# Kernel tuning notes

Hardware: AMD Instinct MI355X
Metric: run time of the kernel (lower is better)

The kernel has to match this reference:

```python
import jax, jax.numpy as jnp
import numpy as np

B, N_GENES, N_SETS, G = 256, 10000, 1000, 128   # batch, input_dim, output_dim, geneset_size
H1, H2 = 64, 32                                  # hidden_dims
EPS = 1e-5                                       # BatchNorm1d eps


def _batchnorm(h, gamma, beta):
    # BatchNorm1d in training mode: biased batch stats over the batch axis
    mean = jnp.mean(h, axis=0, keepdims=True)
    var = jnp.mean(jnp.square(h - mean), axis=0, keepdims=True)
    return (h - mean) * jax.lax.rsqrt(var + EPS) * gamma + beta


def setup_inputs() -> dict:
    key = jax.random.key(0)
    ks = jax.random.split(key, 7)
    # Adjacency with exactly G distinct ones per column -> gather index list [N_SETS, G]
    rng = np.random.default_rng(0)
    gene_idx = np.argsort(rng.random((N_SETS, N_GENES)), axis=1)[:, :G]
    gene_idx = jnp.asarray(np.sort(gene_idx, axis=1), dtype=jnp.int32)

    x = jax.random.normal(ks[0], (B, N_GENES), jnp.float32)
    s1, s2, s3 = 1.0 / np.sqrt(G), 1.0 / np.sqrt(H1), 1.0 / np.sqrt(H2)
    W1 = jax.random.uniform(ks[1], (N_SETS, G, H1), jnp.float32, -s1, s1)
    b1 = jax.random.uniform(ks[2], (N_SETS, H1), jnp.float32, -s1, s1)
    W2 = jax.random.uniform(ks[3], (N_SETS, H1, H2), jnp.float32, -s2, s2)
    b2 = jax.random.uniform(ks[4], (N_SETS, H2), jnp.float32, -s2, s2)
    W3 = jax.random.uniform(ks[5], (N_SETS, H2), jnp.float32, -s3, s3)
    b3 = jax.random.uniform(ks[6], (N_SETS,), jnp.float32, -s3, s3)
    g1 = jnp.ones((N_SETS, H1), jnp.float32)
    be1 = jnp.zeros((N_SETS, H1), jnp.float32)
    g2 = jnp.ones((N_SETS, H2), jnp.float32)
    be2 = jnp.zeros((N_SETS, H2), jnp.float32)
    return {"x": x, "gene_idx": gene_idx, "W1": W1, "b1": b1, "g1": g1, "be1": be1,
            "W2": W2, "b2": b2, "g2": g2, "be2": be2, "W3": W3, "b3": b3}


def reference(x, gene_idx, W1, b1, g1, be1, W2, b2, g2, be2, W3, b3):
    # Per-geneset gather: x[:, adj[:,i]==1] for all i at once -> [B, S, G]
    xg = x[:, gene_idx]
    # Linear -> ReLU -> BatchNorm (per geneset, grouped GEMM)
    h = jax.nn.relu(jnp.einsum('bsg,sgh->bsh', xg, W1) + b1)
    h = _batchnorm(h, g1, be1)
    h = jax.nn.relu(jnp.einsum('bsh,shk->bsk', h, W2) + b2)
    h = _batchnorm(h, g2, be2)
    # Final Linear(H2 -> 1) -> ReLU, concatenated over genesets -> [B, S]
    out = jax.nn.relu(jnp.einsum('bsh,sh->bs', h, W3) + b3)
    return out
```

## Files before the change

kernel.cpp:

```cpp
#include <hip/hip_runtime.h>
#include <stdint.h>

#define BB 256
#define NG 10000
#define NS 1000
#define GG 128
#define H1 64
#define H2 32
#define EPSV 1e-5f


typedef unsigned short ushortT;
typedef __attribute__((ext_vector_type(4))) short short4v;
typedef __attribute__((ext_vector_type(8))) short short8v;
typedef __attribute__((ext_vector_type(4))) float float4v;

__device__ __forceinline__ float bf2f(ushortT u) {
    union { uint32_t i; float f; } v; v.i = ((uint32_t)u) << 16; return v.f;
}
__device__ __forceinline__ ushortT f2bf(float f) {
    union { float f; uint32_t i; } v; v.f = f;
    uint32_t x = v.i;
    return (ushortT)((x + 0x7fffu + ((x >> 16) & 1u)) >> 16);
}
__device__ __forceinline__ uint32_t pack2(ushortT lo, ushortT hi) {
    return (uint32_t)lo | ((uint32_t)hi << 16);
}
__device__ __forceinline__ bool probe_f32(const void* g1) {
    return ((*(const uint32_t*)g1) & 0xFFFFu) == 0u;
}
__device__ __forceinline__ float loadf(const void* p, int i, bool isf) {
    return isf ? ((const float*)p)[i] : bf2f(((const ushortT*)p)[i]);
}
__device__ __forceinline__ ushortT loadbf(const void* p, size_t i, bool isf) {
    return isf ? f2bf(((const float*)p)[i]) : ((const ushortT*)p)[i];
}

__global__ __launch_bounds__(256) void k_transpose(const void* __restrict__ x,
                                                   ushortT* __restrict__ xT,
                                                   const void* __restrict__ g1p) {
    __shared__ ushortT tile[64][66];
    const bool isf = probe_f32(g1p);
    const int tx = threadIdx.x & 63;
    const int tz = threadIdx.x >> 6;
    const int j0 = blockIdx.x * 64;
    const int b0 = blockIdx.y * 64;
    const int j = j0 + tx;
#pragma unroll
    for (int k = 0; k < 16; ++k) {
        int bl = tz * 16 + k;
        ushortT v = 0;
        if (j < NG) v = loadbf(x, (size_t)(b0 + bl) * NG + j, isf);
        tile[bl][tx] = v;
    }
    __syncthreads();
#pragma unroll
    for (int k = 0; k < 16; ++k) {
        int jl = tz * 16 + k;
        int jw = j0 + jl;
        if (jw < NG) xT[jw * BB + b0 + tx] = tile[tx][jl];
    }
}

__global__ __launch_bounds__(256, 4) void k_main(
    const ushortT* __restrict__ xT, const int* __restrict__ gidx,
    const void* __restrict__ W1, const void* __restrict__ W2,
    const void* __restrict__ b1, const void* __restrict__ g1, const void* __restrict__ be1,
    const void* __restrict__ b2, const void* __restrict__ g2, const void* __restrict__ be2,
    const void* __restrict__ W3, const void* __restrict__ b3,
    void* __restrict__ out) {
    __shared__ ushortT xg[BB * 68];
    __shared__ ushortT w1s[64 * 36];

    char* xgc = (char*)xg;
    float* redf = (float*)w1s;
    ushortT* w2s = w1s;

    const bool isf = probe_f32(g1);
    const int s = blockIdx.x;
    const int t = threadIdx.x;
    const int w = t >> 6;
    const int lane = t & 63;
    const int l16 = lane & 15;
    const int quad = lane >> 4;
    const size_t base1 = (size_t)s * (GG * H1);
    const size_t base2 = (size_t)s * (H1 * H2);

#define HOLEI(i)   (*(int*)(xgc + ((i) >> 1) * 136 + 128 + ((i) & 1) * 4))
#define HOLEF(r0, k) (*(float*)(xgc + ((r0) + ((k) >> 1)) * 136 + 128 + ((k) & 1) * 4))

    float b1v[4], w3v[2], b2v[2];
#pragma unroll
    for (int nt = 0; nt < 4; ++nt) b1v[nt] = loadf(b1, s * H1 + nt * 16 + l16, isf);
#pragma unroll
    for (int nt = 0; nt < 2; ++nt) {
        b2v[nt] = loadf(b2, s * H2 + nt * 16 + l16, isf);
        w3v[nt] = loadf(W3, s * H2 + nt * 16 + l16, isf);
    }
    const float b3v = loadf(b3, s, isf);
    float g1v = 0.f, be1v = 0.f, g2v = 0.f, be2v = 0.f;
    if (t < 64) { g1v = loadf(g1, s * H1 + t, isf); be1v = loadf(be1, s * H1 + t, isf); }
    if (t < 32) { g2v = loadf(g2, s * H2 + t, isf); be2v = loadf(be2, s * H2 + t, isf); }

    ushortT w2r[8];
    {
        const int k2 = t & 31, h0 = (t >> 5) * 8;
#pragma unroll
        for (int j = 0; j < 8; ++j) w2r[j] = loadbf(W2, base2 + (size_t)(h0 + j) * H2 + k2, isf);
    }

    if (t < GG) HOLEI(t) = gidx[s * GG + t];

    auto stageW1 = [&](int q) {
#pragma unroll
        for (int rep = 0; rep < 2; ++rep) {
            const int el = rep * 256 + t;
            const int e4 = q * 512 + el;
            const int g = el >> 4;
            const int h0 = (el & 15) * 4;
            ushortT u0, u1, u2, u3;
            if (isf) {
                float4 v = *(const float4*)((const float*)W1 + base1 + (size_t)e4 * 4);
                u0 = f2bf(v.x); u1 = f2bf(v.y); u2 = f2bf(v.z); u3 = f2bf(v.w);
            } else {
                uint2 v = *(const uint2*)((const ushortT*)W1 + base1 + (size_t)e4 * 4);
                u0 = (ushortT)v.x; u1 = (ushortT)(v.x >> 16);
                u2 = (ushortT)v.y; u3 = (ushortT)(v.y >> 16);
            }
            w1s[(h0 + 0) * 36 + g] = u0;
            w1s[(h0 + 1) * 36 + g] = u1;
            w1s[(h0 + 2) * 36 + g] = u2;
            w1s[(h0 + 3) * 36 + g] = u3;
        }
    };
    stageW1(0);
    __syncthreads();

    float4v acc1[4][4];
#pragma unroll
    for (int mt = 0; mt < 4; ++mt)
#pragma unroll
        for (int nt = 0; nt < 4; ++nt) acc1[mt][nt] = (float4v){0.f, 0.f, 0.f, 0.f};

#pragma unroll
    for (int c = 0; c < 2; ++c) {
#pragma unroll
        for (int gq = 0; gq < 8; ++gq) {
            const int i0 = c * 64 + gq * 8;
            int2 p0 = *(const int2*)(xgc + (i0 >> 1) * 136 + 128);
            int2 p1 = *(const int2*)(xgc + ((i0 >> 1) + 1) * 136 + 128);
            int2 p2 = *(const int2*)(xgc + ((i0 >> 1) + 2) * 136 + 128);
            int2 p3 = *(const int2*)(xgc + ((i0 >> 1) + 3) * 136 + 128);
            ushortT v0 = xT[p0.x * BB + t], v1 = xT[p0.y * BB + t];
            ushortT v2 = xT[p1.x * BB + t], v3 = xT[p1.y * BB + t];
            ushortT v4 = xT[p2.x * BB + t], v5 = xT[p2.y * BB + t];
            ushortT v6 = xT[p3.x * BB + t], v7 = xT[p3.y * BB + t];
            uint2 pa = {pack2(v0, v1), pack2(v2, v3)};
            uint2 pb = {pack2(v4, v5), pack2(v6, v7)};
            *(uint2*)(&xg[t * 68 + gq * 8]) = pa;
            *(uint2*)(&xg[t * 68 + gq * 8 + 4]) = pb;
        }
#pragma unroll
        for (int kt = 0; kt < 2; ++kt) {
            const int q = 2 * c + kt;
            if (q > 0) {
                __syncthreads();
                stageW1(q);
                __syncthreads();
            }
            short8v bfrag[4];
#pragma unroll
            for (int nt = 0; nt < 4; ++nt) {
                const int h = nt * 16 + l16;
                const int woff = h * 36 + quad * 8;
                short4v blo = *(const short4v*)(&w1s[woff]);
                short4v bhi = *(const short4v*)(&w1s[woff + 4]);
                bfrag[nt] = __builtin_shufflevector(blo, bhi, 0, 1, 2, 3, 4, 5, 6, 7);
            }
#pragma unroll
            for (int mt = 0; mt < 4; ++mt) {
                const int b = w * 64 + mt * 16 + l16;
                const ushortT* p = &xg[b * 68 + kt * 32 + quad * 8];
                short4v alo = *(const short4v*)(p);
                short4v ahi = *(const short4v*)(p + 4);
                short8v af = __builtin_shufflevector(alo, ahi, 0, 1, 2, 3, 4, 5, 6, 7);
#pragma unroll
                for (int nt = 0; nt < 4; ++nt)
                    acc1[mt][nt] = __builtin_amdgcn_mfma_f32_16x16x32_bf16(af, bfrag[nt], acc1[mt][nt], 0, 0, 0);
            }
        }
    }

    float s1v[4], s2v[4];
#pragma unroll
    for (int nt = 0; nt < 4; ++nt) {
        float s1 = 0.f, s2 = 0.f;
        const float bb = b1v[nt];
#pragma unroll
        for (int mt = 0; mt < 4; ++mt)
#pragma unroll
            for (int r = 0; r < 4; ++r) {
                float v = acc1[mt][nt][r] + bb;
                v = v > 0.f ? v : 0.f;
                s1 += v;
                s2 += v * v;
            }
        s1 += __shfl_xor(s1, 16); s1 += __shfl_xor(s1, 32);
        s2 += __shfl_xor(s2, 16); s2 += __shfl_xor(s2, 32);
        s1v[nt] = s1; s2v[nt] = s2;
    }
    __syncthreads();
    if (lane < 16) {
#pragma unroll
        for (int nt = 0; nt < 4; ++nt) {
            const int k = w * 64 + nt * 16 + lane;
            redf[k] = s1v[nt];
            redf[256 + k] = s2v[nt];
        }
    }
    __syncthreads();

    if (t < 64) {
        float ts = redf[t] + redf[64 + t] + redf[128 + t] + redf[192 + t];
        float tq = redf[256 + t] + redf[320 + t] + redf[384 + t] + redf[448 + t];
        float mean = ts * (1.0f / 256.0f);
        float var = tq * (1.0f / 256.0f) - mean * mean;
        var = var > 0.f ? var : 0.f;
        float rs = rsqrtf(var + EPSV);
        float a = g1v * rs;
        HOLEF(64, t) = a;
        HOLEF(96, t) = be1v - mean * a;
    }
    __syncthreads();

    {
        const int k2 = t & 31, h0 = (t >> 5) * 8;
        uint4 pk;
        pk.x = pack2(w2r[0], w2r[1]);
        pk.y = pack2(w2r[2], w2r[3]);
        pk.z = pack2(w2r[4], w2r[5]);
        pk.w = pack2(w2r[6], w2r[7]);
        *(uint4*)(&w2s[k2 * 72 + h0]) = pk;
    }
#pragma unroll
    for (int nt = 0; nt < 4; ++nt) {
        const int h = nt * 16 + l16;
        const float bb = b1v[nt];
        const float a = HOLEF(64, h), cc = HOLEF(96, h);
#pragma unroll
        for (int mt = 0; mt < 4; ++mt)
#pragma unroll
            for (int r = 0; r < 4; ++r) {
                const int b = w * 64 + mt * 16 + quad * 4 + r;
                float v = acc1[mt][nt][r] + bb;
                v = v > 0.f ? v : 0.f;
                xg[b * 68 + h] = f2bf(v * a + cc);
            }
    }
    __syncthreads();

    float4v acc2[4][2];
#pragma unroll
    for (int mt = 0; mt < 4; ++mt)
#pragma unroll
        for (int nt = 0; nt < 2; ++nt) acc2[mt][nt] = (float4v){0.f, 0.f, 0.f, 0.f};

#pragma unroll
    for (int kt = 0; kt < 2; ++kt) {
        const int kl = kt * 32 + quad * 8;
        short8v bfrag2[2];
#pragma unroll
        for (int nt = 0; nt < 2; ++nt) {
            const int k2 = nt * 16 + l16;
            const int woff = k2 * 72 + kl;
            short4v blo = *(const short4v*)(&w2s[woff]);
            short4v bhi = *(const short4v*)(&w2s[woff + 4]);
            bfrag2[nt] = __builtin_shufflevector(blo, bhi, 0, 1, 2, 3, 4, 5, 6, 7);
        }
#pragma unroll
        for (int mt = 0; mt < 4; ++mt) {
            const int b = w * 64 + mt * 16 + l16;
            const ushortT* p = &xg[b * 68 + kl];
            short4v alo = *(const short4v*)(p);
            short4v ahi = *(const short4v*)(p + 4);
            short8v af = __builtin_shufflevector(alo, ahi, 0, 1, 2, 3, 4, 5, 6, 7);
#pragma unroll
            for (int nt = 0; nt < 2; ++nt)
                acc2[mt][nt] = __builtin_amdgcn_mfma_f32_16x16x32_bf16(af, bfrag2[nt], acc2[mt][nt], 0, 0, 0);
        }
    }

#pragma unroll
    for (int nt = 0; nt < 2; ++nt) {
        float s1 = 0.f, s2 = 0.f;
        const float bb = b2v[nt];
#pragma unroll
        for (int mt = 0; mt < 4; ++mt)
#pragma unroll
            for (int r = 0; r < 4; ++r) {
                float v = acc2[mt][nt][r] + bb;
                v = v > 0.f ? v : 0.f;
                s1 += v;
                s2 += v * v;
            }
        s1 += __shfl_xor(s1, 16); s1 += __shfl_xor(s1, 32);
        s2 += __shfl_xor(s2, 16); s2 += __shfl_xor(s2, 32);
        if (lane < 16) {
            const int k = w * 32 + nt * 16 + lane;
            HOLEF(0, k) = s1;
            HOLEF(64, k) = s2;
        }
    }
    __syncthreads();

    if (t < 32) {
        float ts = HOLEF(0, t) + HOLEF(0, 32 + t) + HOLEF(0, 64 + t) + HOLEF(0, 96 + t);
        float tq = HOLEF(64, t) + HOLEF(64, 32 + t) + HOLEF(64, 64 + t) + HOLEF(64, 96 + t);
        float mean = ts * (1.0f / 256.0f);
        float var = tq * (1.0f / 256.0f) - mean * mean;
        var = var > 0.f ? var : 0.f;
        float rs = rsqrtf(var + EPSV);
        float a = g2v * rs;
        HOLEF(128, t) = a;
        HOLEF(144, t) = be2v - mean * a;
    }
    __syncthreads();

    float a2[2], c2[2];
#pragma unroll
    for (int nt = 0; nt < 2; ++nt) {
        const int k2 = nt * 16 + l16;
        a2[nt] = HOLEF(128, k2);
        c2[nt] = HOLEF(144, k2);
    }
#pragma unroll
    for (int mt = 0; mt < 4; ++mt)
#pragma unroll
        for (int r = 0; r < 4; ++r) {
            float tot = 0.f;
#pragma unroll
            for (int nt = 0; nt < 2; ++nt) {
                float v = acc2[mt][nt][r] + b2v[nt];
                v = v > 0.f ? v : 0.f;
                tot += (v * a2[nt] + c2[nt]) * w3v[nt];
            }
            tot += __shfl_xor(tot, 1);
            tot += __shfl_xor(tot, 2);
            tot += __shfl_xor(tot, 4);
            tot += __shfl_xor(tot, 8);
            if (l16 == 0) {
                const int b = w * 64 + mt * 16 + quad * 4 + r;
                float o = tot + b3v;
                o = o > 0.f ? o : 0.f;
                if (isf) ((float*)out)[b * NS + s] = o;
                else     ((ushortT*)out)[b * NS + s] = f2bf(o);
            }
        }
#undef HOLEI
#undef HOLEF
}

extern "C" void kernel_launch(void* const* d_in, const int* in_sizes, int n_in,
                              void* d_out, int out_size, void* d_ws, size_t ws_size,
                              hipStream_t stream) {
    const int* gi = (const int*)d_in[1];
    ushortT* xT = (ushortT*)d_ws;

    dim3 gT((NG + 63) / 64, BB / 64);
    k_transpose<<<gT, 256, 0, stream>>>(d_in[0], xT, d_in[4]);
    k_main<<<NS, 256, 0, stream>>>(xT, gi, d_in[2], d_in[6],
                                   d_in[3], d_in[4], d_in[5],
                                   d_in[7], d_in[8], d_in[9], d_in[10], d_in[11],
                                   d_out);
}
```

Measured before the change: 142.0 us.

## Vectorize gene gather and prefetch W1 chunks into registers ahead of MFMA

The x gather now has four threads per gene, each doing 16-byte loads of contiguous batch rows from the transposed x. It no longer issues scalar 2-byte loads per thread through gene indices held in LDS, and the results are scattered into the LDS tile. W1 chunks are loaded into registers early and the next chunk is prefetched while the current one is staged, so global latency overlaps with the MFMA work. W2 and BN2 parameter loads move after the first GEMM. The cost is more register pressure and more scalar LDS stores, which may bank-conflict.

```diff
diff --git a/kernel.cpp b/kernel.cpp
--- a/kernel.cpp
+++ b/kernel.cpp
@@ -86,110 +86,161 @@
     const size_t base1 = (size_t)s * (GG * H1);
     const size_t base2 = (size_t)s * (H1 * H2);
 
-#define HOLEI(i)   (*(int*)(xgc + ((i) >> 1) * 136 + 128 + ((i) & 1) * 4))
 #define HOLEF(r0, k) (*(float*)(xgc + ((r0) + ((k) >> 1)) * 136 + 128 + ((k) & 1) * 4))
 
-    float b1v[4], w3v[2], b2v[2];
+    const int gl = t >> 2;
+    const int ml = t & 3;
+    const int gid0 = gidx[s * GG + gl];
+    const int gid1 = gidx[s * GG + 64 + gl];
+
+    const float* W1f = (const float*)W1 + base1;
+    const ushortT* W1h = (const ushortT*)W1 + base1;
+
+    uint4 w1A0, w1A1, w1B0, w1B1;
+    if (isf) {
+        w1A0 = *(const uint4*)(W1f + (size_t)(0 * 512 + 0 * 256 + t) * 4);
+        w1A1 = *(const uint4*)(W1f + (size_t)(0 * 512 + 1 * 256 + t) * 4);
+        w1B0 = *(const uint4*)(W1f + (size_t)(1 * 512 + 0 * 256 + t) * 4);
+        w1B1 = *(const uint4*)(W1f + (size_t)(1 * 512 + 1 * 256 + t) * 4);
+    } else {
+        w1A0 = *(const uint4*)(W1h + (size_t)0 * 2048 + t * 8);
+        w1B0 = *(const uint4*)(W1h + (size_t)1 * 2048 + t * 8);
+    }
+
+    float b1v[4];
 #pragma unroll
     for (int nt = 0; nt < 4; ++nt) b1v[nt] = loadf(b1, s * H1 + nt * 16 + l16, isf);
+    float g1v = 0.f, be1v = 0.f;
+    if (t < 64) { g1v = loadf(g1, s * H1 + t, isf); be1v = loadf(be1, s * H1 + t, isf); }
+
+    auto stageF = [&](uint4 vv, int rr) {
+        union { uint32_t i; float f; } u;
+        const int g = rr * 16 + (t >> 4);
+        const int h0 = (t & 15) * 4;
+        u.i = vv.x; w1s[(h0 + 0) * 36 + g] = f2bf(u.f);
+        u.i = vv.y; w1s[(h0 + 1) * 36 + g] = f2bf(u.f);
+        u.i = vv.z; w1s[(h0 + 2) * 36 + g] = f2bf(u.f);
+        u.i = vv.w; w1s[(h0 + 3) * 36 + g] = f2bf(u.f);
+    };
+    auto stageU = [&](uint4 vv) {
+        const int g = t >> 3;
+        const int h0 = (t & 7) * 8;
+        w1s[(h0 + 0) * 36 + g] = (ushortT)vv.x;
+        w1s[(h0 + 1) * 36 + g] = (ushortT)(vv.x >> 16);
+        w1s[(h0 + 2) * 36 + g] = (ushortT)vv.y;
+        w1s[(h0 + 3) * 36 + g] = (ushortT)(vv.y >> 16);
+        w1s[(h0 + 4) * 36 + g] = (ushortT)vv.z;
+        w1s[(h0 + 5) * 36 + g] = (ushortT)(vv.z >> 16);
+        w1s[(h0 + 6) * 36 + g] = (ushortT)vv.w;
+        w1s[(h0 + 7) * 36 + g] = (ushortT)(vv.w >> 16);
+    };
+
+    float4v acc1[4][4];
+#pragma unroll
+    for (int mt = 0; mt < 4; ++mt)
+#pragma unroll
+        for (int nt = 0; nt < 4; ++nt) acc1[mt][nt] = (float4v){0.f, 0.f, 0.f, 0.f};
+
+    auto mfmaChunk = [&](int kt) {
+        short8v bfrag[4];
+#pragma unroll
+        for (int nt = 0; nt < 4; ++nt) {
+            const int h = nt * 16 + l16;
+            const int woff = h * 36 + quad * 8;
+            short4v blo = *(const short4v*)(&w1s[woff]);
+            short4v bhi = *(const short4v*)(&w1s[woff + 4]);
+            bfrag[nt] = __builtin_shufflevector(blo, bhi, 0, 1, 2, 3, 4, 5, 6, 7);
+        }
+#pragma unroll
+        for (int mt = 0; mt < 4; ++mt) {
+            const int b = w * 64 + mt * 16 + l16;
+            const ushortT* p = &xg[b * 68 + kt * 32 + quad * 8];
+            short4v alo = *(const short4v*)(p);
+            short4v ahi = *(const short4v*)(p + 4);
+            short8v af = __builtin_shufflevector(alo, ahi, 0, 1, 2, 3, 4, 5, 6, 7);
+#pragma unroll
+            for (int nt = 0; nt < 4; ++nt)
+                acc1[mt][nt] = __builtin_amdgcn_mfma_f32_16x16x32_bf16(af, bfrag[nt], acc1[mt][nt], 0, 0, 0);
+        }
+    };
+
+#pragma unroll
+    for (int c = 0; c < 2; ++c) {
+        const int gid = c ? gid1 : gid0;
+        const ushortT* xrow = xT + (size_t)gid * BB;
+        uint4 gv[4];
+#pragma unroll
+        for (int i = 0; i < 4; ++i) gv[i] = *(const uint4*)(xrow + (ml + 4 * i) * 8);
+
+        __syncthreads();
+
+#pragma unroll
+        for (int i = 0; i < 4; ++i) {
+            const int b0 = (ml + 4 * i) * 8;
+            xg[(b0 + 0) * 68 + gl] = (ushortT)gv[i].x;
+            xg[(b0 + 1) * 68 + gl] = (ushortT)(gv[i].x >> 16);
+            xg[(b0 + 2) * 68 + gl] = (ushortT)gv[i].y;
+            xg[(b0 + 3) * 68 + gl] = (ushortT)(gv[i].y >> 16);
+            xg[(b0 + 4) * 68 + gl] = (ushortT)gv[i].z;
+            xg[(b0 + 5) * 68 + gl] = (ushortT)(gv[i].z >> 16);
+            xg[(b0 + 6) * 68 + gl] = (ushortT)gv[i].w;
+            xg[(b0 + 7) * 68 + gl] = (ushortT)(gv[i].w >> 16);
+        }
+#pragma unroll
+        for (int i = 0; i < 4; ++i) gv[i] = *(const uint4*)(xrow + (ml + 4 * i + 16) * 8);
+#pragma unroll
+        for (int i = 0; i < 4; ++i) {
+            const int b0 = (ml + 4 * i + 16) * 8;
+            xg[(b0 + 0) * 68 + gl] = (ushortT)gv[i].x;
+            xg[(b0 + 1) * 68 + gl] = (ushortT)(gv[i].x >> 16);
+            xg[(b0 + 2) * 68 + gl] = (ushortT)gv[i].y;
+            xg[(b0 + 3) * 68 + gl] = (ushortT)(gv[i].y >> 16);
+            xg[(b0 + 4) * 68 + gl] = (ushortT)gv[i].z;
+            xg[(b0 + 5) * 68 + gl] = (ushortT)(gv[i].z >> 16);
+            xg[(b0 + 6) * 68 + gl] = (ushortT)gv[i].w;
+            xg[(b0 + 7) * 68 + gl] = (ushortT)(gv[i].w >> 16);
+        }
+
+        if (isf) { stageF(w1A0, 0); stageF(w1A1, 1); } else { stageU(w1A0); }
+        if (c == 0) {
+            if (isf) {
+                w1A0 = *(const uint4*)(W1f + (size_t)(2 * 512 + 0 * 256 + t) * 4);
+                w1A1 = *(const uint4*)(W1f + (size_t)(2 * 512 + 1 * 256 + t) * 4);
+            } else {
+                w1A0 = *(const uint4*)(W1h + (size_t)2 * 2048 + t * 8);
+            }
+        }
+        __syncthreads();
+        mfmaChunk(0);
+        __syncthreads();
+        if (isf) { stageF(w1B0, 0); stageF(w1B1, 1); } else { stageU(w1B0); }
+        if (c == 0) {
+            if (isf) {
+                w1B0 = *(const uint4*)(W1f + (size_t)(3 * 512 + 0 * 256 + t) * 4);
+                w1B1 = *(const uint4*)(W1f + (size_t)(3 * 512 + 1 * 256 + t) * 4);
+            } else {
+                w1B0 = *(const uint4*)(W1h + (size_t)3 * 2048 + t * 8);
+            }
+        }
+        __syncthreads();
+        mfmaChunk(1);
+    }
+
+    ushortT w2r[8];
+    {
+        const int k2 = t & 31, h0 = (t >> 5) * 8;
+#pragma unroll
+        for (int j = 0; j < 8; ++j) w2r[j] = loadbf(W2, base2 + (size_t)(h0 + j) * H2 + k2, isf);
+    }
+    float b2v[2], w3v[2];
 #pragma unroll
     for (int nt = 0; nt < 2; ++nt) {
         b2v[nt] = loadf(b2, s * H2 + nt * 16 + l16, isf);
         w3v[nt] = loadf(W3, s * H2 + nt * 16 + l16, isf);
     }
     const float b3v = loadf(b3, s, isf);
-    float g1v = 0.f, be1v = 0.f, g2v = 0.f, be2v = 0.f;
-    if (t < 64) { g1v = loadf(g1, s * H1 + t, isf); be1v = loadf(be1, s * H1 + t, isf); }
+    float g2v = 0.f, be2v = 0.f;
     if (t < 32) { g2v = loadf(g2, s * H2 + t, isf); be2v = loadf(be2, s * H2 + t, isf); }
-
-    ushortT w2r[8];
-    {
-        const int k2 = t & 31, h0 = (t >> 5) * 8;
-#pragma unroll
-        for (int j = 0; j < 8; ++j) w2r[j] = loadbf(W2, base2 + (size_t)(h0 + j) * H2 + k2, isf);
-    }
-
-    if (t < GG) HOLEI(t) = gidx[s * GG + t];
-
-    auto stageW1 = [&](int q) {
-#pragma unroll
-        for (int rep = 0; rep < 2; ++rep) {
-            const int el = rep * 256 + t;
-            const int e4 = q * 512 + el;
-            const int g = el >> 4;
-            const int h0 = (el & 15) * 4;
-            ushortT u0, u1, u2, u3;
-            if (isf) {
-                float4 v = *(const float4*)((const float*)W1 + base1 + (size_t)e4 * 4);
-                u0 = f2bf(v.x); u1 = f2bf(v.y); u2 = f2bf(v.z); u3 = f2bf(v.w);
-            } else {
-                uint2 v = *(const uint2*)((const ushortT*)W1 + base1 + (size_t)e4 * 4);
-                u0 = (ushortT)v.x; u1 = (ushortT)(v.x >> 16);
-                u2 = (ushortT)v.y; u3 = (ushortT)(v.y >> 16);
-            }
-            w1s[(h0 + 0) * 36 + g] = u0;
-            w1s[(h0 + 1) * 36 + g] = u1;
-            w1s[(h0 + 2) * 36 + g] = u2;
-            w1s[(h0 + 3) * 36 + g] = u3;
-        }
-    };
-    stageW1(0);
-    __syncthreads();
-
-    float4v acc1[4][4];
-#pragma unroll
-    for (int mt = 0; mt < 4; ++mt)
-#pragma unroll
-        for (int nt = 0; nt < 4; ++nt) acc1[mt][nt] = (float4v){0.f, 0.f, 0.f, 0.f};
-
-#pragma unroll
-    for (int c = 0; c < 2; ++c) {
-#pragma unroll
-        for (int gq = 0; gq < 8; ++gq) {
-            const int i0 = c * 64 + gq * 8;
-            int2 p0 = *(const int2*)(xgc + (i0 >> 1) * 136 + 128);
-            int2 p1 = *(const int2*)(xgc + ((i0 >> 1) + 1) * 136 + 128);
-            int2 p2 = *(const int2*)(xgc + ((i0 >> 1) + 2) * 136 + 128);
-            int2 p3 = *(const int2*)(xgc + ((i0 >> 1) + 3) * 136 + 128);
-            ushortT v0 = xT[p0.x * BB + t], v1 = xT[p0.y * BB + t];
-            ushortT v2 = xT[p1.x * BB + t], v3 = xT[p1.y * BB + t];
-            ushortT v4 = xT[p2.x * BB + t], v5 = xT[p2.y * BB + t];
-            ushortT v6 = xT[p3.x * BB + t], v7 = xT[p3.y * BB + t];
-            uint2 pa = {pack2(v0, v1), pack2(v2, v3)};
-            uint2 pb = {pack2(v4, v5), pack2(v6, v7)};
-            *(uint2*)(&xg[t * 68 + gq * 8]) = pa;
-            *(uint2*)(&xg[t * 68 + gq * 8 + 4]) = pb;
-        }
-#pragma unroll
-        for (int kt = 0; kt < 2; ++kt) {
-            const int q = 2 * c + kt;
-            if (q > 0) {
-                __syncthreads();
-                stageW1(q);
-                __syncthreads();
-            }
-            short8v bfrag[4];
-#pragma unroll
-            for (int nt = 0; nt < 4; ++nt) {
-                const int h = nt * 16 + l16;
-                const int woff = h * 36 + quad * 8;
-                short4v blo = *(const short4v*)(&w1s[woff]);
-                short4v bhi = *(const short4v*)(&w1s[woff + 4]);
-                bfrag[nt] = __builtin_shufflevector(blo, bhi, 0, 1, 2, 3, 4, 5, 6, 7);
-            }
-#pragma unroll
-            for (int mt = 0; mt < 4; ++mt) {
-                const int b = w * 64 + mt * 16 + l16;
-                const ushortT* p = &xg[b * 68 + kt * 32 + quad * 8];
-                short4v alo = *(const short4v*)(p);
-                short4v ahi = *(const short4v*)(p + 4);
-                short8v af = __builtin_shufflevector(alo, ahi, 0, 1, 2, 3, 4, 5, 6, 7);
-#pragma unroll
-                for (int nt = 0; nt < 4; ++nt)
-                    acc1[mt][nt] = __builtin_amdgcn_mfma_f32_16x16x32_bf16(af, bfrag[nt], acc1[mt][nt], 0, 0, 0);
-            }
-        }
-    }
 
     float s1v[4], s2v[4];
 #pragma unroll
@@ -356,7 +407,6 @@
                 else     ((ushortT*)out)[b * NS + s] = f2bf(o);
             }
         }
-#undef HOLEI
 #undef HOLEF
 }
 
```

New measurement: 134.2 us. 1.06x faster.
